# Kernel tuning notes

Measured on AMD Instinct MI355X. Metric: run time of the kernel, lower is better.

Reference implementation:

```python
import jax, jax.numpy as jnp
import numpy as np

B, N_T, D_A, D_V, D_U = 64, 8192, 2, 64, 1
L, MODES, X_PAD = 4, 64, 8


def setup_inputs() -> dict:
    key = jax.random.key(0)
    ks = jax.random.split(key, 9)
    scale = 1.0 / (D_V * D_V)  # Xavier-style gain used in original
    return {
        "v": jax.random.normal(ks[0], (B, N_T), dtype=jnp.float32),
        "grid": jax.random.uniform(ks[1], (N_T,), dtype=jnp.float32),
        "p_w": jax.random.normal(ks[2], (D_A, D_V), dtype=jnp.float32) * 0.1,
        "p_b": jnp.zeros((D_V,), dtype=jnp.float32),
        "fw": jax.random.normal(ks[3], (L, D_V, D_V, MODES, 2), dtype=jnp.float32) * scale,
        "w_w": jax.random.normal(ks[4], (L, D_V, D_V), dtype=jnp.float32) * (1.0 / np.sqrt(D_V)),
        "w_b": jnp.zeros((L, D_V), dtype=jnp.float32),
        "q_w": jax.random.normal(ks[5], (D_V, D_U), dtype=jnp.float32) * (1.0 / np.sqrt(D_V)),
        "q_b": jnp.zeros((D_U,), dtype=jnp.float32),
    }


def _fourier_layer(x, w):
    # x: (B, C, n), w: (C, C, modes, 2) real/imag channel-mixing weights
    n = x.shape[-1]
    xf = jnp.fft.rfft(x)                      # (B, C, n//2+1) complex
    xm = xf[:, :, :MODES]
    xr, xi = jnp.real(xm), jnp.imag(xm)
    wr, wi = w[..., 0], w[..., 1]
    out_r = jnp.einsum('bix,iox->box', xr, wr) - jnp.einsum('bix,iox->box', xi, wi)
    out_i = jnp.einsum('bix,iox->box', xi, wr) + jnp.einsum('bix,iox->box', xr, wi)
    out_m = jax.lax.complex(out_r, out_i)     # (B, C, modes)
    out_ft = jnp.pad(out_m, ((0, 0), (0, 0), (0, n // 2 + 1 - MODES)))
    return jnp.fft.irfft(out_ft, n=n)         # (B, C, n)


def reference(v, grid, p_w, p_b, fw, w_w, w_b, q_w, q_b):
    b, n = v.shape
    # lift: concat signal with coordinate channel -> (B, n, 2)
    x = jnp.concatenate([v[:, :, None], jnp.broadcast_to(grid[None, :, None], (b, n, 1))], axis=-1)
    x = x @ p_w + p_b                          # (B, n, d_v)
    x = jnp.transpose(x, (0, 2, 1))            # (B, d_v, n)
    x = jnp.pad(x, ((0, 0), (0, 0), (0, X_PAD)))
    for i in range(L):
        x1 = _fourier_layer(x, fw[i])
        x2 = jnp.einsum('bcn,cd->bdn', x, w_w[i]) + w_b[i][None, :, None]
        x = x1 + x2
        if i < L - 1:
            x = jax.nn.relu(x)
    x = x[..., :-X_PAD]                        # remove padding
    out = jnp.einsum('bcn,cd->bnd', x, q_w) + q_b  # (B, n, d_u)
    return out[..., 0]                         # d_u == 1 -> squeeze
```

## Files before the change

### kernel.cpp

```cpp
#include <hip/hip_runtime.h>

#define NT    8192
#define NP    8200
#define NPP   8320
#define NB    64
#define DV    64
#define NL    4
#define TFR   520
#define KSP   20
#define SPB   13
#define PI2   6.28318530717958647692f

typedef _Float16 half8 __attribute__((ext_vector_type(8)));
typedef _Float16 half4 __attribute__((ext_vector_type(4)));
typedef float    f32x4 __attribute__((ext_vector_type(4)));

static const size_t B_XT   = 0;
static const size_t B_TABF = 68157440ull;
static const size_t B_TABI = B_TABF + 2129920ull;
static const size_t B_WFR  = B_TABI + 2129920ull;
static const size_t B_ZFR  = B_WFR  + 131072ull;
static const size_t B_XPF  = B_ZFR  + 1048576ull;
static const size_t B_VP   = B_XPF  + 20971520ull;
static const size_t B_G    = B_VP   + 327680ull;
static const size_t B_A    = B_G    + 512ull;

__global__ void k_prep(_Float16* __restrict__ tabF, _Float16* __restrict__ tabI) {
    int idx = blockIdx.x * 256 + threadIdx.x;
    if (idx >= NPP * 64) return;
    int t = idx >> 6, k = idx & 63;
    float c = 0.f, s = 0.f;
    if (t < NP) {
        int m = (int)(((long long)t * (long long)k) % NP);
        float th = (float)m * (PI2 / (float)NP);
        sincosf(th, &s, &c);
    }
    float al = (k == 0) ? (1.f / NP) : (2.f / NP);
    {
        int gs = t >> 5, lh = (t >> 3) & 3, j = t & 7;
        int m0 = 2 * k, m1 = 2 * k + 1;
        tabF[(((size_t)gs * 8 + (m0 >> 4)) * 64 + (m0 & 15) + 16 * lh) * 8 + j] = (_Float16)c;
        tabF[(((size_t)gs * 8 + (m1 >> 4)) * 64 + (m1 & 15) + 16 * lh) * 8 + j] = (_Float16)s;
    }
    {
        int tf = t >> 4, lt = t & 15;
        int m0 = 2 * k, m1 = 2 * k + 1;
        tabI[(((size_t)(m0 >> 5) * TFR + tf) * 64 + lt + 16 * ((m0 >> 3) & 3)) * 8 + (m0 & 7)] = (_Float16)(al * c);
        tabI[(((size_t)(m1 >> 5) * TFR + tf) * 64 + lt + 16 * ((m1 >> 3) & 3)) * 8 + (m1 & 7)] = (_Float16)(al * s);
    }
}

__global__ void k_prep_w(const float* __restrict__ ww, _Float16* __restrict__ Wfrag) {
    int idx = blockIdx.x * 256 + threadIdx.x;
    if (idx >= NL * DV * DV) return;
    int l = idx >> 12, cd = idx & 4095, c = cd >> 6, d = cd & 63;
    float wv = ww[((size_t)l * DV + c) * DV + d];
    _Float16 h = (_Float16)wv;
    _Float16 lo = (_Float16)(wv - (float)h);
    int ks = c >> 5, mf = d >> 4;
    int lane = (d & 15) + 16 * ((c >> 3) & 3), j = c & 7;
    Wfrag[((((size_t)l * 2 + 0) * 2 + ks) * 4 + mf) * 512 + (size_t)lane * 8 + j] = h;
    Wfrag[((((size_t)l * 2 + 1) * 2 + ks) * 4 + mf) * 512 + (size_t)lane * 8 + j] = lo;
}

__global__ void k_prep_p(const float* __restrict__ pw, const float* __restrict__ pb,
                         const float* __restrict__ ww, float* __restrict__ A) {
    int d = threadIdx.x;
    float a0 = 0.f, a1 = 0.f, a2 = 0.f;
    #pragma unroll 8
    for (int c = 0; c < DV; ++c) {
        float w = ww[(size_t)c * DV + d];
        a0 = fmaf(pw[c], w, a0);
        a1 = fmaf(pw[DV + c], w, a1);
        a2 = fmaf(pb[c], w, a2);
    }
    A[d] = a0; A[64 + d] = a1; A[128 + d] = a2;
}

__global__ void k_gd(const float* __restrict__ grd, float* __restrict__ G) {
    __shared__ float rb[256];
    int m = blockIdx.x, k = m >> 1, comp = m & 1;
    int tid = threadIdx.x;
    float s = 0.f;
    for (int t = tid; t < NT; t += 256) {
        int mm = (int)(((long long)t * (long long)k) % NP);
        float th = (float)mm * (PI2 / (float)NP);
        float sn, cs; sincosf(th, &sn, &cs);
        s += grd[t] * (comp ? sn : cs);
    }
    rb[tid] = s; __syncthreads();
    for (int h = 128; h > 0; h >>= 1) { if (tid < h) rb[tid] += rb[tid + h]; __syncthreads(); }
    if (tid == 0) G[m] = rb[0];
}

__launch_bounds__(256)
__global__ void k_fdft_v(const float* __restrict__ v, const _Float16* __restrict__ tabF,
                         _Float16* __restrict__ Vp) {
    int ksb = blockIdx.x;
    int tid = threadIdx.x, w = tid >> 6, lane = tid & 63, g = lane >> 4, r = lane & 15;
    const half8* tFv = (const half8*)tabF;
    f32x4 acc[4][2];
    #pragma unroll
    for (int mf = 0; mf < 4; ++mf)
        #pragma unroll
        for (int nf = 0; nf < 2; ++nf) acc[mf][nf] = (f32x4){0.f, 0.f, 0.f, 0.f};
    for (int s = 0; s < SPB; ++s) {
        int gs = ksb * SPB + s;
        int t0 = gs * 32 + g * 8;
        half8 a[4];
        #pragma unroll
        for (int mf = 0; mf < 4; ++mf) {
            int brow = mf * 16 + r;
            half8 hv;
            if (t0 < NT) {
                const float4* pv = (const float4*)&v[(size_t)brow * NT + t0];
                float4 v0 = pv[0], v1 = pv[1];
                hv[0] = (_Float16)v0.x; hv[1] = (_Float16)v0.y; hv[2] = (_Float16)v0.z; hv[3] = (_Float16)v0.w;
                hv[4] = (_Float16)v1.x; hv[5] = (_Float16)v1.y; hv[6] = (_Float16)v1.z; hv[7] = (_Float16)v1.w;
            } else {
                #pragma unroll
                for (int j = 0; j < 8; ++j) hv[j] = (_Float16)0.f;
            }
            a[mf] = hv;
        }
        half8 bb[2];
        #pragma unroll
        for (int nf = 0; nf < 2; ++nf) bb[nf] = tFv[((size_t)gs * 8 + w * 2 + nf) * 64 + lane];
        #pragma unroll
        for (int mf = 0; mf < 4; ++mf)
            #pragma unroll
            for (int nf = 0; nf < 2; ++nf)
                acc[mf][nf] = __builtin_amdgcn_mfma_f32_16x16x32_f16(a[mf], bb[nf], acc[mf][nf], 0, 0, 0);
    }
    #pragma unroll
    for (int mf = 0; mf < 4; ++mf)
        #pragma unroll
        for (int nf = 0; nf < 2; ++nf)
            #pragma unroll
            for (int reg = 0; reg < 4; ++reg) {
                int brow = mf * 16 + g * 4 + reg;
                int m = w * 32 + nf * 16 + r;
                Vp[((size_t)ksb * NB + brow) * 128 + m] = (_Float16)acc[mf][nf][reg];
            }
}

__launch_bounds__(256)
__global__ void k_fdft(const _Float16* __restrict__ xT, const _Float16* __restrict__ tabF,
                       _Float16* __restrict__ xpf) {
    __shared__ _Float16 xls[2][2048];
    int sb = blockIdx.x, b = blockIdx.y;
    int tid = threadIdx.x, w = tid >> 6, lane = tid & 63, g = lane >> 4, r = lane & 15;
    const half8* tFv = (const half8*)tabF;
    f32x4 acc[4][2];
    #pragma unroll
    for (int cf = 0; cf < 4; ++cf)
        #pragma unroll
        for (int nf = 0; nf < 2; ++nf) acc[cf][nf] = (f32x4){0.f, 0.f, 0.f, 0.f};
    int tl = tid >> 3, c0 = (tid & 7) * 8;

    half8 vv = *(const half8*)&xT[((size_t)b * NPP + (sb * SPB) * 32 + tl) * 64 + c0];
    #pragma unroll
    for (int j = 0; j < 8; ++j) {
        int c = c0 + j;
        xls[0][c * 32 + (tl ^ (((c >> 3) & 3) << 3))] = vv[j];
    }
    int cur = 0;
    #pragma unroll 1
    for (int s = 0; s < SPB; ++s) {
        int gs = sb * SPB + s;
        half8 vvn;
        if (s + 1 < SPB)
            vvn = *(const half8*)&xT[((size_t)b * NPP + (gs + 1) * 32 + tl) * 64 + c0];
        __syncthreads();
        if (s + 1 < SPB) {
            #pragma unroll
            for (int j = 0; j < 8; ++j) {
                int c = c0 + j;
                xls[cur ^ 1][c * 32 + (tl ^ (((c >> 3) & 3) << 3))] = vvn[j];
            }
        }
        half8 a[4], bb[2];
        #pragma unroll
        for (int cf = 0; cf < 4; ++cf) {
            int c = cf * 16 + r;
            a[cf] = *(const half8*)&xls[cur][c * 32 + ((g * 8) ^ ((((c >> 3) & 3)) << 3))];
        }
        #pragma unroll
        for (int nf = 0; nf < 2; ++nf) bb[nf] = tFv[((size_t)gs * 8 + w * 2 + nf) * 64 + lane];
        #pragma unroll
        for (int cf = 0; cf < 4; ++cf)
            #pragma unroll
            for (int nf = 0; nf < 2; ++nf)
                acc[cf][nf] = __builtin_amdgcn_mfma_f32_16x16x32_f16(a[cf], bb[nf], acc[cf][nf], 0, 0, 0);
        cur ^= 1;
    }
    _Float16* xp = xpf + (((size_t)sb * NB + b) * 4 + w) * 2048;
    #pragma unroll
    for (int cf = 0; cf < 4; ++cf)
        #pragma unroll
        for (int nf = 0; nf < 2; ++nf) {
            half4 h4;
            #pragma unroll
            for (int reg = 0; reg < 4; ++reg) h4[reg] = (_Float16)acc[cf][nf][reg];
            *(half4*)&xp[(cf * 2 + nf) * 256 + lane * 4] = h4;
        }
}

__launch_bounds__(256)
__global__ void k_spec0(const _Float16* __restrict__ Vp, const float* __restrict__ G,
                        const float* __restrict__ pw, const float* __restrict__ pb,
                        const float* __restrict__ fw_l, _Float16* __restrict__ zfr) {
    __shared__ float Xs[64][32];
    __shared__ float Vs[32], Gs[32];
    int b = blockIdx.y, kq = blockIdx.x, tid = threadIdx.x;
    if (tid < 32) {
        int m = kq * 32 + tid;
        float ssum = 0.f;
        #pragma unroll
        for (int ks = 0; ks < KSP; ++ks) ssum += (float)Vp[((size_t)ks * NB + b) * 128 + m];
        Vs[tid] = ssum;
        Gs[tid] = G[m];
    }
    __syncthreads();
    #pragma unroll
    for (int q = 0; q < 8; ++q) {
        int flat = q * 256 + tid;
        int i = flat >> 5, ml = flat & 31;
        float xv = pw[i] * Vs[ml] + pw[64 + i] * Gs[ml];
        if (kq == 0 && ml == 0) xv += pb[i] * (float)NT;
        Xs[i][ml] = xv;
    }
    __syncthreads();
    #pragma unroll
    for (int q = 0; q < 4; ++q) {
        int flat = q * 256 + tid;
        int o = flat >> 4, kl = flat & 15;
        int k = kq * 16 + kl;
        float yr = 0.f, yi = 0.f;
        #pragma unroll 8
        for (int i = 0; i < 64; ++i) {
            float2 xv = *(const float2*)&Xs[i][2 * kl];
            float2 wv = *(const float2*)&fw_l[(((size_t)i * DV + o) * 64 + k) * 2];
            yr = fmaf(xv.x, wv.x, fmaf(xv.y, wv.y, yr));
            yi = fmaf(xv.x, wv.y, fmaf(-xv.y, wv.x, yi));
        }
        int mf = o >> 4, mm = 2 * kl, m1 = mm + 1;
        zfr[((((size_t)b * 4 + kq) * 4 + mf) * 64 + (o & 15) + 16 * (mm >> 3)) * 8 + (mm & 7)] = (_Float16)yr;
        zfr[((((size_t)b * 4 + kq) * 4 + mf) * 64 + (o & 15) + 16 * (m1 >> 3)) * 8 + (m1 & 7)] = (_Float16)(-yi);
    }
}

__launch_bounds__(256)
__global__ void k_spec(const _Float16* __restrict__ xpf, const float* __restrict__ fw_l,
                       _Float16* __restrict__ zfr) {
    __shared__ float Xs[64][32];
    int b = blockIdx.y, kq = blockIdx.x, tid = threadIdx.x;
    float a8[8];
    #pragma unroll
    for (int e = 0; e < 8; ++e) a8[e] = 0.f;
    const half8* src = (const half8*)xpf;
    size_t base8 = ((size_t)b * 4 + kq) * 256 + tid;
    const size_t step8 = (size_t)NB * 4 * 256;
    for (int ks = 0; ks < KSP; ++ks) {
        half8 vv = src[base8 + (size_t)ks * step8];
        #pragma unroll
        for (int e = 0; e < 8; ++e) a8[e] += (float)vv[e];
    }
    int cf = tid >> 6, nf2 = (tid >> 5) & 1, lane0 = (tid & 31) * 2;
    #pragma unroll
    for (int e = 0; e < 8; ++e) {
        int lane = lane0 + (e >> 2), reg = e & 3;
        int g = lane >> 4, r = lane & 15;
        Xs[cf * 16 + g * 4 + reg][nf2 * 16 + r] = a8[e];
    }
    __syncthreads();
    #pragma unroll
    for (int q = 0; q < 4; ++q) {
        int flat = q * 256 + tid;
        int o = flat >> 4, kl = flat & 15;
        int k = kq * 16 + kl;
        float yr = 0.f, yi = 0.f;
        #pragma unroll 8
        for (int i = 0; i < 64; ++i) {
            float2 xv = *(const float2*)&Xs[i][2 * kl];
            float2 wv = *(const float2*)&fw_l[(((size_t)i * DV + o) * 64 + k) * 2];
            yr = fmaf(xv.x, wv.x, fmaf(xv.y, wv.y, yr));
            yi = fmaf(xv.x, wv.y, fmaf(-xv.y, wv.x, yi));
        }
        int mf = o >> 4, mm = 2 * kl, m1 = mm + 1;
        zfr[((((size_t)b * 4 + kq) * 4 + mf) * 64 + (o & 15) + 16 * (mm >> 3)) * 8 + (mm & 7)] = (_Float16)yr;
        zfr[((((size_t)b * 4 + kq) * 4 + mf) * 64 + (o & 15) + 16 * (m1 >> 3)) * 8 + (m1 & 7)] = (_Float16)(-yi);
    }
}

template <int MODE>
__launch_bounds__(256)
__global__ void k_inv(const _Float16* __restrict__ zfr, const _Float16* __restrict__ tabI,
                      const _Float16* __restrict__ Wl, const float* __restrict__ wb_l,
                      const float* __restrict__ qw, const float* __restrict__ qb,
                      const float* __restrict__ v, const float* __restrict__ grd,
                      const float* __restrict__ A,
                      _Float16* __restrict__ xT, float* __restrict__ out) {
    __shared__ _Float16 xw[4][2048];
    __shared__ float Asm[3][64];
    int b = blockIdx.y, ksb = blockIdx.x;
    int tid = threadIdx.x, w = tid >> 6, lane = tid & 63;
    int g = lane >> 4, r = lane & 15;
    int tw = ksb * 128 + w * 32;
    const half8* zfv = (const half8*)zfr;
    const half8* tIv = (const half8*)tabI;
    const half8* wfv = (const half8*)Wl;

    if (MODE == 0) {
        if (tid < 192) Asm[tid >> 6][tid & 63] = A[tid];
        __syncthreads();
    }

    f32x4 acc[4][2];
    #pragma unroll
    for (int mf = 0; mf < 4; ++mf)
        #pragma unroll
        for (int nf = 0; nf < 2; ++nf) acc[mf][nf] = (f32x4){0.f, 0.f, 0.f, 0.f};

    #pragma unroll
    for (int ks4 = 0; ks4 < 4; ++ks4) {
        half8 az[4], bt[2];
        #pragma unroll
        for (int mf = 0; mf < 4; ++mf)
            az[mf] = zfv[(((size_t)b * 4 + ks4) * 4 + mf) * 64 + lane];
        #pragma unroll
        for (int nf = 0; nf < 2; ++nf)
            bt[nf] = tIv[((size_t)ks4 * TFR + (tw >> 4) + nf) * 64 + lane];
        #pragma unroll
        for (int mf = 0; mf < 4; ++mf)
            #pragma unroll
            for (int nf = 0; nf < 2; ++nf)
                acc[mf][nf] = __builtin_amdgcn_mfma_f32_16x16x32_f16(az[mf], bt[nf], acc[mf][nf], 0, 0, 0);
    }
    if (MODE != 0) {
        half8 xb[2][2];
        #pragma unroll
        for (int ks = 0; ks < 2; ++ks)
            #pragma unroll
            for (int nf = 0; nf < 2; ++nf)
                xb[ks][nf] = *(const half8*)&xT[((size_t)b * NPP + tw + nf * 16 + r) * 64 + ks * 32 + g * 8];
        #pragma unroll
        for (int hl = 0; hl < 2; ++hl)
            #pragma unroll
            for (int ks = 0; ks < 2; ++ks) {
                half8 aw[4];
                #pragma unroll
                for (int mf = 0; mf < 4; ++mf)
                    aw[mf] = wfv[((size_t)(hl * 2 + ks) * 4 + mf) * 64 + lane];
                #pragma unroll
                for (int mf = 0; mf < 4; ++mf)
                    #pragma unroll
                    for (int nf = 0; nf < 2; ++nf)
                        acc[mf][nf] = __builtin_amdgcn_mfma_f32_16x16x32_f16(aw[mf], xb[ks][nf], acc[mf][nf], 0, 0, 0);
            }
    }

    if (MODE != 2) {
        float vv[2], gg[2];
        if (MODE == 0) {
            #pragma unroll
            for (int nf = 0; nf < 2; ++nf) {
                int t = tw + nf * 16 + r;
                bool in = (t < NT);
                vv[nf] = in ? v[(size_t)b * NT + t] : 0.f;
                gg[nf] = in ? grd[t] : 0.f;
            }
        }
        #pragma unroll
        for (int mf = 0; mf < 4; ++mf)
            #pragma unroll
            for (int nf = 0; nf < 2; ++nf) {
                int tl = nf * 16 + r;
                half4 h4;
                #pragma unroll
                for (int reg = 0; reg < 4; ++reg) {
                    int o = mf * 16 + g * 4 + reg;
                    float val = acc[mf][nf][reg] + wb_l[o];
                    if (MODE == 0)
                        val += fmaf(Asm[0][o], vv[nf], fmaf(Asm[1][o], gg[nf], Asm[2][o]));
                    h4[reg] = (_Float16)fmaxf(val, 0.f);
                }
                int idx = tl * 64 + ((mf * 16 + g * 4) ^ ((tl & 7) << 3));
                *(half4*)&xw[w][idx] = h4;
            }
        #pragma unroll
        for (int it = 0; it < 4; ++it) {
            int t = it * 8 + (lane >> 3);
            int cg = lane & 7;
            half8 vv8 = *(const half8*)&xw[w][t * 64 + ((cg * 8) ^ ((t & 7) << 3))];
            *(half8*)&xT[((size_t)b * NPP + tw + t) * 64 + cg * 8] = vv8;
        }
    } else {
        float p0 = 0.f, p1 = 0.f;
        #pragma unroll
        for (int mf = 0; mf < 4; ++mf)
            #pragma unroll
            for (int reg = 0; reg < 4; ++reg) {
                int o = mf * 16 + g * 4 + reg;
                float qq = qw[o], bias = wb_l[o];
                p0 = fmaf(acc[mf][0][reg] + bias, qq, p0);
                p1 = fmaf(acc[mf][1][reg] + bias, qq, p1);
            }
        p0 += __shfl_xor(p0, 16); p0 += __shfl_xor(p0, 32);
        p1 += __shfl_xor(p1, 16); p1 += __shfl_xor(p1, 32);
        float qbv = qb[0];
        if (g == 0) out[(size_t)b * NT + tw + r]      = p0 + qbv;
        if (g == 1) out[(size_t)b * NT + tw + 16 + r] = p1 + qbv;
    }
}

extern "C" void kernel_launch(void* const* d_in, const int* in_sizes, int n_in,
                              void* d_out, int out_size, void* d_ws, size_t ws_size,
                              hipStream_t stream) {
    const float* v   = (const float*)d_in[0];
    const float* grd = (const float*)d_in[1];
    const float* pw  = (const float*)d_in[2];
    const float* pb  = (const float*)d_in[3];
    const float* fw  = (const float*)d_in[4];
    const float* ww  = (const float*)d_in[5];
    const float* wb  = (const float*)d_in[6];
    const float* qw  = (const float*)d_in[7];
    const float* qb  = (const float*)d_in[8];
    float* out = (float*)d_out;

    char* wsb = (char*)d_ws;
    _Float16* xT    = (_Float16*)(wsb + B_XT);
    _Float16* tabFb = (_Float16*)(wsb + B_TABF);
    _Float16* tabIb = (_Float16*)(wsb + B_TABI);
    _Float16* Wfrag = (_Float16*)(wsb + B_WFR);
    _Float16* zfrag = (_Float16*)(wsb + B_ZFR);
    _Float16* xpf   = (_Float16*)(wsb + B_XPF);
    _Float16* Vpart = (_Float16*)(wsb + B_VP);
    float*    G     = (float*)(wsb + B_G);
    float*    A     = (float*)(wsb + B_A);

    k_prep<<<(NPP * 64 + 255) / 256, 256, 0, stream>>>(tabFb, tabIb);
    k_prep_w<<<(NL * DV * DV + 255) / 256, 256, 0, stream>>>(ww, Wfrag);
    k_prep_p<<<1, 64, 0, stream>>>(pw, pb, ww, A);
    k_gd<<<128, 256, 0, stream>>>(grd, G);
    k_fdft_v<<<KSP, 256, 0, stream>>>(v, tabFb, Vpart);

    for (int l = 0; l < NL; ++l) {
        if (l == 0) {
            k_spec0<<<dim3(4, NB), 256, 0, stream>>>(Vpart, G, pw, pb, fw, zfrag);
        } else {
            k_fdft<<<dim3(KSP, NB), 256, 0, stream>>>(xT, tabFb, xpf);
            k_spec<<<dim3(4, NB), 256, 0, stream>>>(xpf, fw + (size_t)l * DV * DV * 64 * 2, zfrag);
        }
        const _Float16* wf_l = Wfrag + (size_t)l * 8192;
        const float* wb_l = wb + (size_t)l * DV;
        if (l == 0)
            k_inv<0><<<dim3(NPP / 128, NB), 256, 0, stream>>>(
                zfrag, tabIb, wf_l, wb_l, qw, qb, v, grd, A, xT, out);
        else if (l < NL - 1)
            k_inv<1><<<dim3(NPP / 128, NB), 256, 0, stream>>>(
                zfrag, tabIb, wf_l, wb_l, qw, qb, v, grd, A, xT, out);
        else
            k_inv<2><<<dim3(NT / 128, NB), 256, 0, stream>>>(
                zfrag, tabIb, wf_l, wb_l, qw, qb, v, grd, A, xT, out);
    }
}
```

Baseline: 301.2 us.

## Launch inverse-DFT kernel as single-wave blocks and vectorize table prep stores

The inverse transform kernel is relaunched with one 64-thread wavefront per block instead of four per block. Each block uses a quarter of the LDS and needs no block barrier, which is meant to improve scheduling flexibility and occupancy. The twiddle-table prep kernel is restructured so each thread computes eight table entries and writes them as one contiguous half8 store instead of scattered 2-byte stores. In exchange, prep does more sincos work per thread and the inverse kernel launches more, smaller blocks.

Result: no change. 297.2 us (-1.3%).

```diff
diff --git a/kernel.cpp b/kernel.cpp
--- a/kernel.cpp
+++ b/kernel.cpp
@@ -27,26 +27,49 @@
 
 __global__ void k_prep(_Float16* __restrict__ tabF, _Float16* __restrict__ tabI) {
     int idx = blockIdx.x * 256 + threadIdx.x;
-    if (idx >= NPP * 64) return;
-    int t = idx >> 6, k = idx & 63;
-    float c = 0.f, s = 0.f;
-    if (t < NP) {
-        int m = (int)(((long long)t * (long long)k) % NP);
-        float th = (float)m * (PI2 / (float)NP);
-        sincosf(th, &s, &c);
-    }
-    float al = (k == 0) ? (1.f / NP) : (2.f / NP);
-    {
-        int gs = t >> 5, lh = (t >> 3) & 3, j = t & 7;
-        int m0 = 2 * k, m1 = 2 * k + 1;
-        tabF[(((size_t)gs * 8 + (m0 >> 4)) * 64 + (m0 & 15) + 16 * lh) * 8 + j] = (_Float16)c;
-        tabF[(((size_t)gs * 8 + (m1 >> 4)) * 64 + (m1 & 15) + 16 * lh) * 8 + j] = (_Float16)s;
-    }
-    {
-        int tf = t >> 4, lt = t & 15;
-        int m0 = 2 * k, m1 = 2 * k + 1;
-        tabI[(((size_t)(m0 >> 5) * TFR + tf) * 64 + lt + 16 * ((m0 >> 3) & 3)) * 8 + (m0 & 7)] = (_Float16)(al * c);
-        tabI[(((size_t)(m1 >> 5) * TFR + tf) * 64 + lt + 16 * ((m1 >> 3) & 3)) * 8 + (m1 & 7)] = (_Float16)(al * s);
+    if (idx < 133120) {
+        int lane = idx & 63;
+        int rest = idx >> 6;
+        int cf = rest & 7, gs = rest >> 3;
+        int ml = lane & 15, lh = lane >> 4;
+        int m = cf * 16 + ml, k = m >> 1, comp = m & 1;
+        half8 o;
+        #pragma unroll
+        for (int j = 0; j < 8; ++j) {
+            int t = gs * 32 + lh * 8 + j;
+            float val = 0.f;
+            if (t < NP) {
+                int mm = (int)(((long long)t * (long long)k) % NP);
+                float th = (float)mm * (PI2 / (float)NP);
+                float sn, cs; sincosf(th, &sn, &cs);
+                val = comp ? sn : cs;
+            }
+            o[j] = (_Float16)val;
+        }
+        *(half8*)&tabF[(size_t)idx * 8] = o;
+    } else if (idx < 266240) {
+        int id2 = idx - 133120;
+        int lane = id2 & 63;
+        int rest = id2 >> 6;
+        int tf = rest % 520, ks = rest / 520;
+        int lt = lane & 15, mh = lane >> 4;
+        int t = tf * 16 + lt;
+        half8 o;
+        #pragma unroll
+        for (int j = 0; j < 8; ++j) {
+            int m = ks * 32 + mh * 8 + j;
+            int k = m >> 1, comp = m & 1;
+            float val = 0.f;
+            if (t < NP) {
+                int mm = (int)(((long long)t * (long long)k) % NP);
+                float th = (float)mm * (PI2 / (float)NP);
+                float sn, cs; sincosf(th, &sn, &cs);
+                float al = (k == 0) ? (1.f / NP) : (2.f / NP);
+                val = al * (comp ? sn : cs);
+            }
+            o[j] = (_Float16)val;
+        }
+        *(half8*)&tabI[(size_t)id2 * 8] = o;
     }
 }
 
@@ -294,17 +317,19 @@
 }
 
 template <int MODE>
-__launch_bounds__(256)
+__launch_bounds__(64)
 __global__ void k_inv(const _Float16* __restrict__ zfr, const _Float16* __restrict__ tabI,
                       const _Float16* __restrict__ Wl, const float* __restrict__ wb_l,
                       const float* __restrict__ qw, const float* __restrict__ qb,
                       const float* __restrict__ v, const float* __restrict__ grd,
                       const float* __restrict__ A,
                       _Float16* __restrict__ xT, float* __restrict__ out) {
-    __shared__ _Float16 xw[4][2048];
+    __shared__ _Float16 xw[2048];
     __shared__ float Asm[3][64];
-    int b = blockIdx.y, ksb = blockIdx.x;
-    int tid = threadIdx.x, w = tid >> 6, lane = tid & 63;
+    int b = blockIdx.y;
+    int wid = blockIdx.x;
+    int ksb = wid >> 2, w = wid & 3;
+    int lane = threadIdx.x;
     int g = lane >> 4, r = lane & 15;
     int tw = ksb * 128 + w * 32;
     const half8* zfv = (const half8*)zfr;
@@ -312,8 +337,9 @@
     const half8* wfv = (const half8*)Wl;
 
     if (MODE == 0) {
-        if (tid < 192) Asm[tid >> 6][tid & 63] = A[tid];
-        __syncthreads();
+        Asm[0][lane] = A[lane];
+        Asm[1][lane] = A[64 + lane];
+        Asm[2][lane] = A[128 + lane];
     }
 
     f32x4 acc[4][2];
@@ -386,13 +412,13 @@
                     h4[reg] = (_Float16)fmaxf(val, 0.f);
                 }
                 int idx = tl * 64 + ((mf * 16 + g * 4) ^ ((tl & 7) << 3));
-                *(half4*)&xw[w][idx] = h4;
+                *(half4*)&xw[idx] = h4;
             }
         #pragma unroll
         for (int it = 0; it < 4; ++it) {
             int t = it * 8 + (lane >> 3);
             int cg = lane & 7;
-            half8 vv8 = *(const half8*)&xw[w][t * 64 + ((cg * 8) ^ ((t & 7) << 3))];
+            half8 vv8 = *(const half8*)&xw[t * 64 + ((cg * 8) ^ ((t & 7) << 3))];
             *(half8*)&xT[((size_t)b * NPP + tw + t) * 64 + cg * 8] = vv8;
         }
     } else {
@@ -439,7 +465,7 @@
     float*    G     = (float*)(wsb + B_G);
     float*    A     = (float*)(wsb + B_A);
 
-    k_prep<<<(NPP * 64 + 255) / 256, 256, 0, stream>>>(tabFb, tabIb);
+    k_prep<<<1040, 256, 0, stream>>>(tabFb, tabIb);
     k_prep_w<<<(NL * DV * DV + 255) / 256, 256, 0, stream>>>(ww, Wfrag);
     k_prep_p<<<1, 64, 0, stream>>>(pw, pb, ww, A);
     k_gd<<<128, 256, 0, stream>>>(grd, G);
@@ -455,13 +481,13 @@
         const _Float16* wf_l = Wfrag + (size_t)l * 8192;
         const float* wb_l = wb + (size_t)l * DV;
         if (l == 0)
-            k_inv<0><<<dim3(NPP / 128, NB), 256, 0, stream>>>(
+            k_inv<0><<<dim3(260, NB), 64, 0, stream>>>(
                 zfrag, tabIb, wf_l, wb_l, qw, qb, v, grd, A, xT, out);
         else if (l < NL - 1)
-            k_inv<1><<<dim3(NPP / 128, NB), 256, 0, stream>>>(
+            k_inv<1><<<dim3(260, NB), 64, 0, stream>>>(
                 zfrag, tabIb, wf_l, wb_l, qw, qb, v, grd, A, xT, out);
         else
-            k_inv<2><<<dim3(NT / 128, NB), 256, 0, stream>>>(
+            k_inv<2><<<dim3(256, NB), 64, 0, stream>>>(
                 zfrag, tabIb, wf_l, wb_l, qw, qb, v, grd, A, xT, out);
     }
 }
```
